# Kernel optimization log

Hardware: AMD Instinct MI355X
Metric: run time of the kernel (lower is better)

The kernel has to match this reference:

```python
import jax, jax.numpy as jnp
import numpy as np

ROUTINGS = 3

def squash(t, axis=-1):
    s2 = jnp.sum(jnp.square(t), axis=axis, keepdims=True)
    safe_norm = jnp.sqrt(s2 + 1e-7)
    scale = s2 / (1.0 + s2)
    return scale * (t / safe_norm)

def setup_inputs() -> dict:
    key = jax.random.key(0)
    k1, k2 = jax.random.split(key)
    B, I, K = 64, 2048, 8      # batch, input_num_caps, input_dim_caps
    J, L = 32, 16              # num_caps, dim_caps
    inputs = jax.random.normal(k1, (B, I, K), dtype=jnp.float32)
    # glorot-uniform-ish init for W [I, J, K, L]
    limit = np.sqrt(6.0 / (K + L)).astype(np.float32)
    W = jax.random.uniform(k2, (I, J, K, L), dtype=jnp.float32, minval=-limit, maxval=limit)
    return {"inputs": inputs, "W": W}

def reference(inputs, W):
    # uji: predicted capsules [B, I, J, L]
    uji = jnp.einsum('ijkl,bik->bijl', W, inputs)
    B, I, J, _ = uji.shape
    b = jnp.zeros((B, I, J, 1), dtype=uji.dtype)
    vj = None
    for _ in range(ROUTINGS):
        cj = jax.nn.softmax(b, axis=-1)          # size-1 axis -> all ones (faithful)
        s = jnp.sum(cj * uji, axis=1, keepdims=True)  # [B, 1, J, L]
        s = s[..., None]                          # [B, 1, J, L, 1]
        vj = squash(s, axis=-2)                   # squash over L
        # agreement: contract over L (k) and trailing size-1 axis (z)
        agreement = jnp.einsum('bijk,bmjkz->bijm', uji, vj)  # [B, I, J, 1]
        b = b + agreement
    return vj
```

## Files before the change

### kernel.cpp

```cpp
#include <hip/hip_runtime.h>
#include <hip/hip_bf16.h>
#include <stdint.h>


using f32x4 = __attribute__((ext_vector_type(4))) float;
using s16x8 = __attribute__((ext_vector_type(8))) short;

__device__ __forceinline__ short f2bf(float x) {
    __hip_bfloat16 h = __float2bfloat16(x);
    return *reinterpret_cast<short*>(&h);
}
__device__ __forceinline__ float bf2f(short s) {
    return __uint_as_float(((uint32_t)(uint16_t)s) << 16);
}

struct WBuf { float v[2][8];   };
struct IBuf { f32x4 v[4][2];   };

template<int KSPLITS>
__global__ __launch_bounds__(256)
void caps_gemm(const float* __restrict__ In, const float* __restrict__ W,
               float* __restrict__ ws)
{
    constexpr int KS    = 16384 / KSPLITS;
    constexpr int NSTEP = KS / 32;

    const int tid  = threadIdx.x;
    const int wv   = tid >> 6;
    const int lane = tid & 63;
    const int q    = lane >> 4;
    const int cin  = lane & 15;
    const int kb0  = blockIdx.x * KS;
    const int c0   = blockIdx.y * 128 + wv * 32;

    f32x4 acc[4][2] = {};

    auto load_step = [&](int s, WBuf& wb, IBuf& ib) {
        const int kb = kb0 + s * 32;
        const int i0 = (kb >> 3) + q;
        #pragma unroll
        for (int nt = 0; nt < 2; ++nt) {
            const int c = c0 + nt * 16 + cin;
            const float* wp = W + (size_t)i0 * 4096 + (c >> 4) * 128 + (c & 15);
            #pragma unroll
            for (int e = 0; e < 8; ++e) wb.v[nt][e] = wp[e * 16];
        }
        #pragma unroll
        for (int mt = 0; mt < 4; ++mt) {
            const float* ip = In + (size_t)(mt * 16 + cin) * 16384 + kb + q * 8;
            ib.v[mt][0] = *(const f32x4*)(ip);
            ib.v[mt][1] = *(const f32x4*)(ip + 4);
        }
    };

    auto compute = [&](const WBuf& wb, const IBuf& ib) {
        s16x8 Ah[4], Al[4], Bh[2], Bl[2];
        #pragma unroll
        for (int mt = 0; mt < 4; ++mt)
            #pragma unroll
            for (int e = 0; e < 8; ++e) {
                float x = ib.v[mt][e >> 2][e & 3];
                short h = f2bf(x);
                Ah[mt][e] = h;
                Al[mt][e] = f2bf(x - bf2f(h));
            }
        #pragma unroll
        for (int nt = 0; nt < 2; ++nt)
            #pragma unroll
            for (int e = 0; e < 8; ++e) {
                float x = wb.v[nt][e];
                short h = f2bf(x);
                Bh[nt][e] = h;
                Bl[nt][e] = f2bf(x - bf2f(h));
            }
        #pragma unroll
        for (int mt = 0; mt < 4; ++mt)
            #pragma unroll
            for (int nt = 0; nt < 2; ++nt) {
                acc[mt][nt] = __builtin_amdgcn_mfma_f32_16x16x32_bf16(Ah[mt], Bh[nt], acc[mt][nt], 0, 0, 0);
                acc[mt][nt] = __builtin_amdgcn_mfma_f32_16x16x32_bf16(Al[mt], Bh[nt], acc[mt][nt], 0, 0, 0);
                acc[mt][nt] = __builtin_amdgcn_mfma_f32_16x16x32_bf16(Ah[mt], Bl[nt], acc[mt][nt], 0, 0, 0);
            }
    };

    WBuf wA, wB;
    IBuf iA, iB;
    load_step(0, wA, iA);
    #pragma unroll 1
    for (int ss = 0; ss < NSTEP; ss += 2) {
        load_step(ss + 1, wB, iB);
        compute(wA, iA);
        if (ss + 2 < NSTEP) load_step(ss + 2, wA, iA);
        compute(wB, iB);
    }

    float* wsb = ws + (size_t)blockIdx.x * 32768;
    #pragma unroll
    for (int mt = 0; mt < 4; ++mt)
        #pragma unroll
        for (int nt = 0; nt < 2; ++nt) {
            const int c = c0 + nt * 16 + cin;
            #pragma unroll
            for (int r = 0; r < 4; ++r)
                wsb[(mt * 16 + q * 4 + r) * 512 + c] = acc[mt][nt][r];
        }
}

__global__ __launch_bounds__(256)
void caps_finish(const float* __restrict__ ws, float* __restrict__ out, int nk)
{
    const int o = blockIdx.x * 256 + threadIdx.x;
    float s = 0.0f;
    #pragma unroll 8
    for (int ks = 0; ks < nk; ++ks) s += ws[(size_t)ks * 32768 + o];
    float s2 = s * s;
    s2 += __shfl_xor(s2, 1);
    s2 += __shfl_xor(s2, 2);
    s2 += __shfl_xor(s2, 4);
    s2 += __shfl_xor(s2, 8);
    const float scale = s2 / (1.0f + s2);
    out[o] = s * scale / sqrtf(s2 + 1e-7f);
}

extern "C" void kernel_launch(void* const* d_in, const int* in_sizes, int n_in,
                              void* d_out, int out_size, void* d_ws, size_t ws_size,
                              hipStream_t stream)
{
    (void)in_sizes; (void)n_in; (void)out_size;
    const float* In = (const float*)d_in[0];
    const float* W  = (const float*)d_in[1];
    float* out = (float*)d_out;
    float* ws  = (float*)d_ws;

    const size_t slab = 32768u * sizeof(float);
    if (ws_size >= 128 * slab) {
        caps_gemm<128><<<dim3(128, 4), dim3(256), 0, stream>>>(In, W, ws);
        caps_finish<<<dim3(128), dim3(256), 0, stream>>>(ws, out, 128);
    } else if (ws_size >= 64 * slab) {
        caps_gemm<64><<<dim3(64, 4), dim3(256), 0, stream>>>(In, W, ws);
        caps_finish<<<dim3(128), dim3(256), 0, stream>>>(ws, out, 64);
    } else if (ws_size >= 8 * slab) {
        caps_gemm<8><<<dim3(8, 4), dim3(256), 0, stream>>>(In, W, ws);
        caps_finish<<<dim3(128), dim3(256), 0, stream>>>(ws, out, 8);
    } else {
        caps_gemm<1><<<dim3(1, 4), dim3(256), 0, stream>>>(In, W, out);
        caps_finish<<<dim3(128), dim3(256), 0, stream>>>(out, out, 1);
    }
}
```

Measured before the change: 93.20 us.

## Stage W tiles into LDS via async global_load_lds with double buffering

W is no longer fetched with strided scalar global loads per lane. Each block now copies a contiguous 4-capsule W tile into a double-buffered LDS array using global_load_lds 16-byte transfers, and lanes read their B fragments from LDS, with barriers between stages. The finish kernel also gets 8 independent partial accumulators so the split-K reduction has more loads in flight. This trades the uncoalesced global W traffic for LDS reads, which may hit bank conflicts, plus two block-wide syncs per step pair.

```diff
diff --git a/kernel.cpp b/kernel.cpp
--- a/kernel.cpp
+++ b/kernel.cpp
@@ -5,6 +5,9 @@
 
 using f32x4 = __attribute__((ext_vector_type(4))) float;
 using s16x8 = __attribute__((ext_vector_type(8))) short;
+
+typedef __attribute__((address_space(3))) uint32_t lds_u32;
+typedef const __attribute__((address_space(1))) uint32_t glb_u32;
 
 __device__ __forceinline__ short f2bf(float x) {
     __hip_bfloat16 h = __float2bfloat16(x);
@@ -14,8 +17,7 @@
     return __uint_as_float(((uint32_t)(uint16_t)s) << 16);
 }
 
-struct WBuf { float v[2][8];   };
-struct IBuf { f32x4 v[4][2];   };
+struct IBuf { f32x4 v[4][2]; };
 
 template<int KSPLITS>
 __global__ __launch_bounds__(256)
@@ -31,20 +33,28 @@
     const int q    = lane >> 4;
     const int cin  = lane & 15;
     const int kb0  = blockIdx.x * KS;
+    const int j0   = blockIdx.y * 8;
     const int c0   = blockIdx.y * 128 + wv * 32;
+
+    __shared__ float wlds[2][4096];
+
+    const int s_jj = tid >> 5, s_k = (tid >> 2) & 7, s_l4 = tid & 3;
+    const float* wsrc0 = W + (size_t)(j0 + s_jj) * 128 + s_k * 16 + s_l4 * 4;
 
     f32x4 acc[4][2] = {};
 
-    auto load_step = [&](int s, WBuf& wb, IBuf& ib) {
+    auto stage_w = [&](int s, int b) {
+        const int i0s = (kb0 >> 3) + s * 4;
+        #pragma unroll
+        for (int n = 0; n < 4; ++n) {
+            const float* gp = wsrc0 + (size_t)(i0s + n) * 4096;
+            float* lp = &wlds[b][n * 1024 + wv * 256];
+            __builtin_amdgcn_global_load_lds((glb_u32*)gp, (lds_u32*)lp, 16, 0, 0);
+        }
+    };
+
+    auto load_in = [&](int s, IBuf& ib) {
         const int kb = kb0 + s * 32;
-        const int i0 = (kb >> 3) + q;
-        #pragma unroll
-        for (int nt = 0; nt < 2; ++nt) {
-            const int c = c0 + nt * 16 + cin;
-            const float* wp = W + (size_t)i0 * 4096 + (c >> 4) * 128 + (c & 15);
-            #pragma unroll
-            for (int e = 0; e < 8; ++e) wb.v[nt][e] = wp[e * 16];
-        }
         #pragma unroll
         for (int mt = 0; mt < 4; ++mt) {
             const float* ip = In + (size_t)(mt * 16 + cin) * 16384 + kb + q * 8;
@@ -53,8 +63,20 @@
         }
     };
 
-    auto compute = [&](const WBuf& wb, const IBuf& ib) {
-        s16x8 Ah[4], Al[4], Bh[2], Bl[2];
+    auto compute = [&](int b, const IBuf& ib) {
+        s16x8 Bh[2], Bl[2];
+        #pragma unroll
+        for (int nt = 0; nt < 2; ++nt) {
+            const int jjf = wv * 2 + nt;
+            #pragma unroll
+            for (int e = 0; e < 8; ++e) {
+                float x = wlds[b][q * 1024 + jjf * 128 + e * 16 + cin];
+                short h = f2bf(x);
+                Bh[nt][e] = h;
+                Bl[nt][e] = f2bf(x - bf2f(h));
+            }
+        }
+        s16x8 Ah[4], Al[4];
         #pragma unroll
         for (int mt = 0; mt < 4; ++mt)
             #pragma unroll
@@ -63,15 +85,6 @@
                 short h = f2bf(x);
                 Ah[mt][e] = h;
                 Al[mt][e] = f2bf(x - bf2f(h));
-            }
-        #pragma unroll
-        for (int nt = 0; nt < 2; ++nt)
-            #pragma unroll
-            for (int e = 0; e < 8; ++e) {
-                float x = wb.v[nt][e];
-                short h = f2bf(x);
-                Bh[nt][e] = h;
-                Bl[nt][e] = f2bf(x - bf2f(h));
             }
         #pragma unroll
         for (int mt = 0; mt < 4; ++mt)
@@ -83,15 +96,18 @@
             }
     };
 
-    WBuf wA, wB;
     IBuf iA, iB;
-    load_step(0, wA, iA);
+    stage_w(0, 0);
+    load_in(0, iA);
+    __syncthreads();
     #pragma unroll 1
     for (int ss = 0; ss < NSTEP; ss += 2) {
-        load_step(ss + 1, wB, iB);
-        compute(wA, iA);
-        if (ss + 2 < NSTEP) load_step(ss + 2, wA, iA);
-        compute(wB, iB);
+        if (ss + 1 < NSTEP) { stage_w(ss + 1, 1); load_in(ss + 1, iB); }
+        compute(0, iA);
+        __syncthreads();
+        if (ss + 2 < NSTEP) { stage_w(ss + 2, 0); load_in(ss + 2, iA); }
+        if (ss + 1 < NSTEP) compute(1, iB);
+        __syncthreads();
     }
 
     float* wsb = ws + (size_t)blockIdx.x * 32768;
@@ -111,8 +127,18 @@
 {
     const int o = blockIdx.x * 256 + threadIdx.x;
     float s = 0.0f;
-    #pragma unroll 8
-    for (int ks = 0; ks < nk; ++ks) s += ws[(size_t)ks * 32768 + o];
+    if (nk >= 8) {
+        float a[8] = {};
+        #pragma unroll 1
+        for (int ks = 0; ks < nk; ks += 8)
+            #pragma unroll
+            for (int u = 0; u < 8; ++u)
+                a[u] += ws[(size_t)(ks + u) * 32768 + o];
+        #pragma unroll
+        for (int u = 0; u < 8; ++u) s += a[u];
+    } else {
+        for (int ks = 0; ks < nk; ++ks) s += ws[(size_t)ks * 32768 + o];
+    }
     float s2 = s * s;
     s2 += __shfl_xor(s2, 1);
     s2 += __shfl_xor(s2, 2);
```

New measurement: 94.19 us. No clear change (+1.1%).

## Pre-split inputs to bf16 hi/lo and reduce split-K partials with atomics

Applied to the files above, without the earlier changes.

Adds a prep kernel that converts the fp32 inputs once into bf16 hi/lo planes and zeroes the accumulator. The GEMM then reads the bf16 planes directly, so each block no longer repeats the conversion. The GEMM is re-tiled to one output capsule per wave with 64 K-splits, and the partial sums go to a single slab through atomicAdd instead of 128 partial slabs. That removes the large workspace write and the reduction pass. The cost is an extra kernel launch, atomic contention, and non-deterministic summation order.

```diff
diff --git a/kernel.cpp b/kernel.cpp
--- a/kernel.cpp
+++ b/kernel.cpp
@@ -4,6 +4,7 @@
 
 
 using f32x4 = __attribute__((ext_vector_type(4))) float;
+using s16x4 = __attribute__((ext_vector_type(4))) short;
 using s16x8 = __attribute__((ext_vector_type(8))) short;
 
 __device__ __forceinline__ short f2bf(float x) {
@@ -14,105 +15,96 @@
     return __uint_as_float(((uint32_t)(uint16_t)s) << 16);
 }
 
-struct WBuf { float v[2][8];   };
-struct IBuf { f32x4 v[4][2];   };
-
-template<int KSPLITS>
-__global__ __launch_bounds__(256)
-void caps_gemm(const float* __restrict__ In, const float* __restrict__ W,
-               float* __restrict__ ws)
-{
-    constexpr int KS    = 16384 / KSPLITS;
-    constexpr int NSTEP = KS / 32;
-
-    const int tid  = threadIdx.x;
-    const int wv   = tid >> 6;
-    const int lane = tid & 63;
-    const int q    = lane >> 4;
-    const int cin  = lane & 15;
-    const int kb0  = blockIdx.x * KS;
-    const int c0   = blockIdx.y * 128 + wv * 32;
-
-    f32x4 acc[4][2] = {};
-
-    auto load_step = [&](int s, WBuf& wb, IBuf& ib) {
-        const int kb = kb0 + s * 32;
-        const int i0 = (kb >> 3) + q;
-        #pragma unroll
-        for (int nt = 0; nt < 2; ++nt) {
-            const int c = c0 + nt * 16 + cin;
-            const float* wp = W + (size_t)i0 * 4096 + (c >> 4) * 128 + (c & 15);
-            #pragma unroll
-            for (int e = 0; e < 8; ++e) wb.v[nt][e] = wp[e * 16];
-        }
+
+__global__ __launch_bounds__(256)
+void caps_prep(const float* __restrict__ In, float* __restrict__ ws)
+{
+    const int g = blockIdx.x * 256 + threadIdx.x;
+    short* hi = (short*)(ws + 32768);
+    short* lo = hi + (1 << 20);
+    f32x4 v = *(const f32x4*)(In + (size_t)g * 4);
+    s16x4 h4, l4;
+    #pragma unroll
+    for (int e = 0; e < 4; ++e) {
+        short h = f2bf(v[e]);
+        h4[e] = h;
+        l4[e] = f2bf(v[e] - bf2f(h));
+    }
+    *(s16x4*)(hi + (size_t)g * 4) = h4;
+    *(s16x4*)(lo + (size_t)g * 4) = l4;
+    if (blockIdx.x < 128) ws[blockIdx.x * 256 + threadIdx.x] = 0.0f;
+}
+
+struct WReg { float v[8]; };
+struct AReg { s16x8 h[4], l[4]; };
+
+__global__ __launch_bounds__(256)
+void caps_gemm_at(const float* __restrict__ W, float* __restrict__ ws)
+{
+    const int tid = threadIdx.x, wv = tid >> 6, lane = tid & 63;
+    const int q = lane >> 4, cin = lane & 15;
+    const int kb0 = blockIdx.x * 256;
+    const int j   = blockIdx.y * 4 + wv;
+    const short* hi = (const short*)(ws + 32768);
+    const short* lo = hi + (1 << 20);
+    const float* wbase = W + (size_t)j * 128 + cin;
+
+    f32x4 acc[4] = {};
+
+    auto load_step = [&](int s, WReg& wr, AReg& ar) {
+        const int i0 = (kb0 >> 3) + s * 4 + q;
+        const float* wp = wbase + (size_t)i0 * 4096;
+        #pragma unroll
+        for (int e = 0; e < 8; ++e) wr.v[e] = wp[e * 16];
+        const int kb = kb0 + s * 32 + q * 8;
         #pragma unroll
         for (int mt = 0; mt < 4; ++mt) {
-            const float* ip = In + (size_t)(mt * 16 + cin) * 16384 + kb + q * 8;
-            ib.v[mt][0] = *(const f32x4*)(ip);
-            ib.v[mt][1] = *(const f32x4*)(ip + 4);
+            const size_t o = (size_t)(mt * 16 + cin) * 16384 + kb;
+            ar.h[mt] = *(const s16x8*)(hi + o);
+            ar.l[mt] = *(const s16x8*)(lo + o);
         }
     };
 
-    auto compute = [&](const WBuf& wb, const IBuf& ib) {
-        s16x8 Ah[4], Al[4], Bh[2], Bl[2];
-        #pragma unroll
-        for (int mt = 0; mt < 4; ++mt)
-            #pragma unroll
-            for (int e = 0; e < 8; ++e) {
-                float x = ib.v[mt][e >> 2][e & 3];
-                short h = f2bf(x);
-                Ah[mt][e] = h;
-                Al[mt][e] = f2bf(x - bf2f(h));
-            }
-        #pragma unroll
-        for (int nt = 0; nt < 2; ++nt)
-            #pragma unroll
-            for (int e = 0; e < 8; ++e) {
-                float x = wb.v[nt][e];
-                short h = f2bf(x);
-                Bh[nt][e] = h;
-                Bl[nt][e] = f2bf(x - bf2f(h));
-            }
-        #pragma unroll
-        for (int mt = 0; mt < 4; ++mt)
-            #pragma unroll
-            for (int nt = 0; nt < 2; ++nt) {
-                acc[mt][nt] = __builtin_amdgcn_mfma_f32_16x16x32_bf16(Ah[mt], Bh[nt], acc[mt][nt], 0, 0, 0);
-                acc[mt][nt] = __builtin_amdgcn_mfma_f32_16x16x32_bf16(Al[mt], Bh[nt], acc[mt][nt], 0, 0, 0);
-                acc[mt][nt] = __builtin_amdgcn_mfma_f32_16x16x32_bf16(Ah[mt], Bl[nt], acc[mt][nt], 0, 0, 0);
-            }
+    auto compute = [&](const WReg& wr, const AReg& ar) {
+        s16x8 Bh, Bl;
+        #pragma unroll
+        for (int e = 0; e < 8; ++e) {
+            short h = f2bf(wr.v[e]);
+            Bh[e] = h;
+            Bl[e] = f2bf(wr.v[e] - bf2f(h));
+        }
+        #pragma unroll
+        for (int mt = 0; mt < 4; ++mt) {
+            acc[mt] = __builtin_amdgcn_mfma_f32_16x16x32_bf16(ar.h[mt], Bh, acc[mt], 0, 0, 0);
+            acc[mt] = __builtin_amdgcn_mfma_f32_16x16x32_bf16(ar.l[mt], Bh, acc[mt], 0, 0, 0);
+            acc[mt] = __builtin_amdgcn_mfma_f32_16x16x32_bf16(ar.h[mt], Bl, acc[mt], 0, 0, 0);
+        }
     };
 
-    WBuf wA, wB;
-    IBuf iA, iB;
-    load_step(0, wA, iA);
+    WReg wA, wB; AReg aA, aB;
+    load_step(0, wA, aA);
     #pragma unroll 1
-    for (int ss = 0; ss < NSTEP; ss += 2) {
-        load_step(ss + 1, wB, iB);
-        compute(wA, iA);
-        if (ss + 2 < NSTEP) load_step(ss + 2, wA, iA);
-        compute(wB, iB);
-    }
-
-    float* wsb = ws + (size_t)blockIdx.x * 32768;
+    for (int ss = 0; ss < 8; ss += 2) {
+        load_step(ss + 1, wB, aB);
+        compute(wA, aA);
+        if (ss + 2 < 8) load_step(ss + 2, wA, aA);
+        compute(wB, aB);
+    }
+
     #pragma unroll
-    for (int mt = 0; mt < 4; ++mt)
-        #pragma unroll
-        for (int nt = 0; nt < 2; ++nt) {
-            const int c = c0 + nt * 16 + cin;
-            #pragma unroll
-            for (int r = 0; r < 4; ++r)
-                wsb[(mt * 16 + q * 4 + r) * 512 + c] = acc[mt][nt][r];
-        }
-}
-
-__global__ __launch_bounds__(256)
-void caps_finish(const float* __restrict__ ws, float* __restrict__ out, int nk)
+    for (int mt = 0; mt < 4; ++mt) {
+        const int b = mt * 16 + q * 4;
+        #pragma unroll
+        for (int r = 0; r < 4; ++r)
+            atomicAdd(ws + (b + r) * 512 + j * 16 + cin, acc[mt][r]);
+    }
+}
+
+__global__ __launch_bounds__(256)
+void caps_squash(const float* __restrict__ ws, float* __restrict__ out)
 {
     const int o = blockIdx.x * 256 + threadIdx.x;
-    float s = 0.0f;
-    #pragma unroll 8
-    for (int ks = 0; ks < nk; ++ks) s += ws[(size_t)ks * 32768 + o];
+    float s = ws[o];
     float s2 = s * s;
     s2 += __shfl_xor(s2, 1);
     s2 += __shfl_xor(s2, 2);
@@ -122,6 +114,81 @@
     out[o] = s * scale / sqrtf(s2 + 1e-7f);
 }
 
+__global__ __launch_bounds__(256)
+void caps_gemm_direct(const float* __restrict__ In, const float* __restrict__ W,
+                      float* __restrict__ outp)
+{
+    const int tid = threadIdx.x, wv = tid >> 6, lane = tid & 63;
+    const int q = lane >> 4, cin = lane & 15;
+    const int c0 = blockIdx.y * 128 + wv * 32;
+    f32x4 acc[4][2] = {};
+    #pragma unroll 1
+    for (int ssk = 0; ssk < 512; ++ssk) {
+        const int kb = ssk * 32;
+        const int i0 = (kb >> 3) + q;
+        float wvv[2][8];
+        s16x8 Ah[4], Al[4];
+        #pragma unroll
+        for (int nt = 0; nt < 2; ++nt) {
+            const int c = c0 + nt * 16 + cin;
+            const float* wp = W + (size_t)i0 * 4096 + (c >> 4) * 128 + (c & 15);
+            #pragma unroll
+            for (int e = 0; e < 8; ++e) wvv[nt][e] = wp[e * 16];
+        }
+        #pragma unroll
+        for (int mt = 0; mt < 4; ++mt) {
+            const float* ip = In + (size_t)(mt * 16 + cin) * 16384 + kb + q * 8;
+            #pragma unroll
+            for (int e = 0; e < 8; ++e) {
+                float x = ip[e];
+                short h = f2bf(x);
+                Ah[mt][e] = h;
+                Al[mt][e] = f2bf(x - bf2f(h));
+            }
+        }
+        #pragma unroll
+        for (int nt = 0; nt < 2; ++nt) {
+            s16x8 Bh, Bl;
+            #pragma unroll
+            for (int e = 0; e < 8; ++e) {
+                float x = wvv[nt][e];
+                short h = f2bf(x);
+                Bh[e] = h;
+                Bl[e] = f2bf(x - bf2f(h));
+            }
+            #pragma unroll
+            for (int mt = 0; mt < 4; ++mt) {
+                acc[mt][nt] = __builtin_amdgcn_mfma_f32_16x16x32_bf16(Ah[mt], Bh, acc[mt][nt], 0, 0, 0);
+                acc[mt][nt] = __builtin_amdgcn_mfma_f32_16x16x32_bf16(Al[mt], Bh, acc[mt][nt], 0, 0, 0);
+                acc[mt][nt] = __builtin_amdgcn_mfma_f32_16x16x32_bf16(Ah[mt], Bl, acc[mt][nt], 0, 0, 0);
+            }
+        }
+    }
+    #pragma unroll
+    for (int mt = 0; mt < 4; ++mt)
+        #pragma unroll
+        for (int nt = 0; nt < 2; ++nt) {
+            const int c = c0 + nt * 16 + cin;
+            #pragma unroll
+            for (int r = 0; r < 4; ++r)
+                outp[(mt * 16 + q * 4 + r) * 512 + c] = acc[mt][nt][r];
+        }
+}
+
+__global__ __launch_bounds__(256)
+void caps_squash_inplace(float* __restrict__ out)
+{
+    const int o = blockIdx.x * 256 + threadIdx.x;
+    float s = out[o];
+    float s2 = s * s;
+    s2 += __shfl_xor(s2, 1);
+    s2 += __shfl_xor(s2, 2);
+    s2 += __shfl_xor(s2, 4);
+    s2 += __shfl_xor(s2, 8);
+    const float scale = s2 / (1.0f + s2);
+    out[o] = s * scale / sqrtf(s2 + 1e-7f);
+}
+
 extern "C" void kernel_launch(void* const* d_in, const int* in_sizes, int n_in,
                               void* d_out, int out_size, void* d_ws, size_t ws_size,
                               hipStream_t stream)
@@ -132,18 +199,13 @@
     float* out = (float*)d_out;
     float* ws  = (float*)d_ws;
 
-    const size_t slab = 32768u * sizeof(float);
-    if (ws_size >= 128 * slab) {
-        caps_gemm<128><<<dim3(128, 4), dim3(256), 0, stream>>>(In, W, ws);
-        caps_finish<<<dim3(128), dim3(256), 0, stream>>>(ws, out, 128);
-    } else if (ws_size >= 64 * slab) {
-        caps_gemm<64><<<dim3(64, 4), dim3(256), 0, stream>>>(In, W, ws);
-        caps_finish<<<dim3(128), dim3(256), 0, stream>>>(ws, out, 64);
-    } else if (ws_size >= 8 * slab) {
-        caps_gemm<8><<<dim3(8, 4), dim3(256), 0, stream>>>(In, W, ws);
-        caps_finish<<<dim3(128), dim3(256), 0, stream>>>(ws, out, 8);
+    const size_t need = 32768u * sizeof(float) + (2u << 20) * sizeof(short) * 2;
+    if (ws_size >= need) {
+        caps_prep    <<<dim3(1024),     dim3(256), 0, stream>>>(In, ws);
+        caps_gemm_at <<<dim3(64, 8),    dim3(256), 0, stream>>>(W, ws);
+        caps_squash  <<<dim3(128),      dim3(256), 0, stream>>>(ws, out);
     } else {
-        caps_gemm<1><<<dim3(1, 4), dim3(256), 0, stream>>>(In, W, out);
-        caps_finish<<<dim3(128), dim3(256), 0, stream>>>(out, out, 1);
-    }
-}
+        caps_gemm_direct   <<<dim3(1, 4), dim3(256), 0, stream>>>(In, W, out);
+        caps_squash_inplace<<<dim3(128),  dim3(256), 0, stream>>>(out);
+    }
+}
```

Measured after the change: 99.99 us. 7.3% more time.
